# Kernel optimization log

Measured on AMD Instinct MI355X. Metric: run time of the kernel, lower is better.

Reference implementation:

```python
import jax, jax.numpy as jnp
import numpy as np

NUM_NODES = 50000

def setup_inputs() -> dict:
    key = jax.random.key(0)
    k1, k2 = jax.random.split(key)
    x = jax.random.normal(k1, (NUM_NODES, 64), dtype=jnp.float32)
    edge_index = jax.random.randint(k2, (2, 800000), 0, NUM_NODES, dtype=jnp.int64)
    return {"x": x, "edge_index": edge_index}

def reference(x, edge_index):
    # gather source-node features along edges, scatter-mean into target nodes
    row, col = edge_index[0], edge_index[1]
    num_nodes = x.shape[0]
    gathered = x[row]  # [E, D]
    summed = jax.ops.segment_sum(gathered, col, num_segments=num_nodes)  # [N, D]
    count = jax.ops.segment_sum(jnp.ones_like(col, dtype=x.dtype), col, num_segments=num_nodes)  # [N]
    # mean with divide-by-zero guard (matches torch_geometric scatter reduce='mean')
    out = summed / jnp.maximum(count, 1.0)[:, None]
    return out
```

## Files before the change

### kernel.cpp

```cpp
#include <hip/hip_runtime.h>

#define N_NODES 50000
#define DIM 64
#define NPB 32
#define NB 1563
#define NCHUNK 128
#define CAPB 1024
#define CAP 1024

typedef unsigned short ushort_t;

__device__ __forceinline__ ushort_t f32_to_bf16(float f) {
    unsigned u = __float_as_uint(f);
    u += 0x7FFFu + ((u >> 16) & 1u);
    return (ushort_t)(u >> 16);
}

__device__ __forceinline__ void acc_pair(float& a0, float& a1, unsigned u) {
    a0 += __uint_as_float(u << 16);
    a1 += __uint_as_float(u & 0xFFFF0000u);
}

__global__ void convert_hist_kernel(const float* __restrict__ xf,
                                    ushort_t* __restrict__ xh,
                                    const int* __restrict__ col,
                                    int* __restrict__ localH,
                                    int E, int chunk, int n4) {
    __shared__ int h[NB];
    int c = blockIdx.x;
    int tid = threadIdx.x;
    for (int i = c * blockDim.x + tid; i < n4; i += gridDim.x * blockDim.x) {
        float4 v = *reinterpret_cast<const float4*>(xf + (size_t)i * 4);
        ushort4 hh;
        hh.x = f32_to_bf16(v.x);
        hh.y = f32_to_bf16(v.y);
        hh.z = f32_to_bf16(v.z);
        hh.w = f32_to_bf16(v.w);
        *reinterpret_cast<ushort4*>(xh + (size_t)i * 4) = hh;
    }
    for (int b = tid; b < NB; b += blockDim.x) h[b] = 0;
    __syncthreads();
    int beg = c * chunk, end = min(beg + chunk, E);
    int nfull = (end - beg) >> 2;
    for (int g = tid; g < nfull; g += blockDim.x) {
        int4 c4 = *reinterpret_cast<const int4*>(col + beg + g * 4);
        atomicAdd(&h[c4.x >> 5], 1);
        atomicAdd(&h[c4.y >> 5], 1);
        atomicAdd(&h[c4.z >> 5], 1);
        atomicAdd(&h[c4.w >> 5], 1);
    }
    for (int e = beg + nfull * 4 + tid; e < end; e += blockDim.x)
        atomicAdd(&h[col[e] >> 5], 1);
    __syncthreads();
    for (int b = tid; b < NB; b += blockDim.x)
        localH[(size_t)c * NB + b] = h[b];
}

__global__ void chunk_offset_kernel(int* __restrict__ localH,
                                    int* __restrict__ bucket_total) {
    int b = blockIdx.x;
    int lane = threadIdx.x;
    int running = 0;
    #pragma unroll
    for (int c0 = 0; c0 < NCHUNK; c0 += 64) {
        int c = c0 + lane;
        int v = localH[(size_t)c * NB + b];
        int incl = v;
        #pragma unroll
        for (int ofs = 1; ofs < 64; ofs <<= 1) {
            int t = __shfl_up(incl, ofs);
            if (lane >= ofs) incl += t;
        }
        localH[(size_t)c * NB + b] = running + incl - v;
        running += __shfl(incl, 63);
    }
    if (lane == 0) bucket_total[b] = running;
}

__global__ void binning_kernel(const int* __restrict__ row,
                               const int* __restrict__ col,
                               const int* __restrict__ localH,
                               unsigned* __restrict__ packed,
                               int E, int chunk) {
    __shared__ int cursor[NB];
    int c = blockIdx.x;
    int tid = threadIdx.x;
    for (int b = tid; b < NB; b += blockDim.x)
        cursor[b] = b * CAPB + localH[(size_t)c * NB + b];
    __syncthreads();
    int beg = c * chunk, end = min(beg + chunk, E);
    int nfull = (end - beg) >> 2;
    for (int g = tid; g < nfull; g += blockDim.x) {
        int e = beg + g * 4;
        int4 d4 = *reinterpret_cast<const int4*>(col + e);
        int4 s4 = *reinterpret_cast<const int4*>(row + e);
        int p0 = atomicAdd(&cursor[d4.x >> 5], 1);
        packed[p0] = (unsigned)s4.x | ((unsigned)(d4.x & 31) << 16);
        int p1 = atomicAdd(&cursor[d4.y >> 5], 1);
        packed[p1] = (unsigned)s4.y | ((unsigned)(d4.y & 31) << 16);
        int p2 = atomicAdd(&cursor[d4.z >> 5], 1);
        packed[p2] = (unsigned)s4.z | ((unsigned)(d4.z & 31) << 16);
        int p3 = atomicAdd(&cursor[d4.w >> 5], 1);
        packed[p3] = (unsigned)s4.w | ((unsigned)(d4.w & 31) << 16);
    }
    for (int e = beg + nfull * 4 + tid; e < end; e += blockDim.x) {
        int d = col[e];
        int p = atomicAdd(&cursor[d >> 5], 1);
        packed[p] = (unsigned)row[e] | ((unsigned)(d & 31) << 16);
    }
}

template <bool BF16>
__global__ __launch_bounds__(512)
void aggregate_bucket_kernel(const float* __restrict__ xf,
                             const ushort_t* __restrict__ xh,
                             const unsigned* __restrict__ packed,
                             const int* __restrict__ bucket_total,
                             float* __restrict__ out) {
    __shared__ unsigned buf[CAP];
    __shared__ unsigned short srcs[CAP];
    __shared__ int hist[NPB];
    __shared__ int segoff[NPB];
    __shared__ int cursor[NPB];
    __shared__ int cnt_tot[NPB];

    int b = blockIdx.x;
    int tid = threadIdx.x;
    int lane = tid & 63;
    int wv = tid >> 6;
    int g8 = lane >> 3;
    int o = lane & 7;
    int seg_beg = b * CAPB;
    int seg_end = seg_beg + bucket_total[b];
    int node_base = b * NPB;
    int nnodes = min(NPB, N_NODES - node_base);

    float acc[4][8];
    #pragma unroll
    for (int r = 0; r < 4; ++r)
        #pragma unroll
        for (int k = 0; k < 8; ++k) acc[r][k] = 0.0f;
    if (tid < NPB) cnt_tot[tid] = 0;

    for (int cs = seg_beg; cs < seg_end; cs += CAP) {
        int m = min(CAP, seg_end - cs);
        __syncthreads();
        if (tid < NPB) hist[tid] = 0;
        __syncthreads();
        for (int i = tid; i < m; i += 512) {
            unsigned v = packed[cs + i];
            buf[i] = v;
            atomicAdd(&hist[v >> 16], 1);
        }
        __syncthreads();
        if (tid < NPB) {
            int v = hist[tid];
            int incl = v;
            #pragma unroll
            for (int ofs = 1; ofs < 32; ofs <<= 1) {
                int t = __shfl_up(incl, ofs);
                if (lane >= ofs) incl += t;
            }
            segoff[tid] = incl - v;
            cursor[tid] = incl - v;
            cnt_tot[tid] += v;
        }
        __syncthreads();
        for (int i = tid; i < m; i += 512) {
            unsigned v = buf[i];
            int p = atomicAdd(&cursor[v >> 16], 1);
            srcs[p] = (unsigned short)(v & 0xFFFF);
        }
        __syncthreads();
        #pragma unroll
        for (int r = 0; r < 4; ++r) {
            int ln = wv * 4 + r;
            int st = segoff[ln];
            int len = hist[ln];
            int j = 0;
            for (; j + 16 <= len; j += 16) {
                int s0 = srcs[st + j + g8];
                int s1 = srcs[st + j + 8 + g8];
                if (BF16) {
                    uint4 a0 = *reinterpret_cast<const uint4*>(xh + (size_t)s0 * DIM + o * 8);
                    uint4 a1 = *reinterpret_cast<const uint4*>(xh + (size_t)s1 * DIM + o * 8);
                    acc_pair(acc[r][0], acc[r][1], a0.x);
                    acc_pair(acc[r][2], acc[r][3], a0.y);
                    acc_pair(acc[r][4], acc[r][5], a0.z);
                    acc_pair(acc[r][6], acc[r][7], a0.w);
                    acc_pair(acc[r][0], acc[r][1], a1.x);
                    acc_pair(acc[r][2], acc[r][3], a1.y);
                    acc_pair(acc[r][4], acc[r][5], a1.z);
                    acc_pair(acc[r][6], acc[r][7], a1.w);
                } else {
                    float4 u0 = *reinterpret_cast<const float4*>(xf + (size_t)s0 * DIM + o * 8);
                    float4 u1 = *reinterpret_cast<const float4*>(xf + (size_t)s0 * DIM + o * 8 + 4);
                    float4 u2 = *reinterpret_cast<const float4*>(xf + (size_t)s1 * DIM + o * 8);
                    float4 u3 = *reinterpret_cast<const float4*>(xf + (size_t)s1 * DIM + o * 8 + 4);
                    acc[r][0] += u0.x + u2.x; acc[r][1] += u0.y + u2.y;
                    acc[r][2] += u0.z + u2.z; acc[r][3] += u0.w + u2.w;
                    acc[r][4] += u1.x + u3.x; acc[r][5] += u1.y + u3.y;
                    acc[r][6] += u1.z + u3.z; acc[r][7] += u1.w + u3.w;
                }
            }
            for (; j < len; j += 8) {
                if (j + g8 < len) {
                    int s = srcs[st + j + g8];
                    if (BF16) {
                        uint4 a0 = *reinterpret_cast<const uint4*>(xh + (size_t)s * DIM + o * 8);
                        acc_pair(acc[r][0], acc[r][1], a0.x);
                        acc_pair(acc[r][2], acc[r][3], a0.y);
                        acc_pair(acc[r][4], acc[r][5], a0.z);
                        acc_pair(acc[r][6], acc[r][7], a0.w);
                    } else {
                        float4 u0 = *reinterpret_cast<const float4*>(xf + (size_t)s * DIM + o * 8);
                        float4 u1 = *reinterpret_cast<const float4*>(xf + (size_t)s * DIM + o * 8 + 4);
                        acc[r][0] += u0.x; acc[r][1] += u0.y;
                        acc[r][2] += u0.z; acc[r][3] += u0.w;
                        acc[r][4] += u1.x; acc[r][5] += u1.y;
                        acc[r][6] += u1.z; acc[r][7] += u1.w;
                    }
                }
            }
        }
    }
    __syncthreads();
    #pragma unroll
    for (int r = 0; r < 4; ++r) {
        int ln = wv * 4 + r;
        #pragma unroll
        for (int k = 0; k < 8; ++k) {
            acc[r][k] += __shfl_xor(acc[r][k], 8);
            acc[r][k] += __shfl_xor(acc[r][k], 16);
            acc[r][k] += __shfl_xor(acc[r][k], 32);
        }
        if (g8 == 0 && ln < nnodes) {
            int c = cnt_tot[ln];
            float inv = (c > 0) ? 1.0f / (float)c : 0.0f;
            float4 lo = make_float4(acc[r][0] * inv, acc[r][1] * inv,
                                    acc[r][2] * inv, acc[r][3] * inv);
            float4 hi = make_float4(acc[r][4] * inv, acc[r][5] * inv,
                                    acc[r][6] * inv, acc[r][7] * inv);
            float* op = out + (size_t)(node_base + ln) * DIM + o * 8;
            *reinterpret_cast<float4*>(op) = lo;
            *reinterpret_cast<float4*>(op + 4) = hi;
        }
    }
}

extern "C" void kernel_launch(void* const* d_in, const int* in_sizes, int n_in,
                              void* d_out, int out_size, void* d_ws, size_t ws_size,
                              hipStream_t stream) {
    const float* x = (const float*)d_in[0];
    const int* edge_index = (const int*)d_in[1];
    int E = in_sizes[1] / 2;
    const int* row = edge_index;
    const int* col = edge_index + E;
    float* out = (float*)d_out;

    int chunk = (((E + NCHUNK - 1) / NCHUNK) + 3) & ~3;
    int n4 = N_NODES * DIM / 4;

    int* bucket_total = (int*)d_ws;
    int* localH       = bucket_total + 1568;
    unsigned* packed  = (unsigned*)(localH + (size_t)NCHUNK * NB);
    ushort_t* xh      = (ushort_t*)(packed + (size_t)NB * CAPB);
    size_t need_bf16  = (size_t)((char*)(xh + (size_t)N_NODES * DIM) - (char*)d_ws);
    bool use_bf16 = (ws_size >= need_bf16);

    convert_hist_kernel<<<NCHUNK, 1024, 0, stream>>>(x, xh, col, localH, E, chunk,
                                                     use_bf16 ? n4 : 0);
    chunk_offset_kernel<<<NB, 64, 0, stream>>>(localH, bucket_total);
    binning_kernel<<<NCHUNK, 1024, 0, stream>>>(row, col, localH, packed, E, chunk);
    if (use_bf16)
        aggregate_bucket_kernel<true><<<NB, 512, 0, stream>>>(x, xh, packed, bucket_total, out);
    else
        aggregate_bucket_kernel<false><<<NB, 512, 0, stream>>>(x, xh, packed, bucket_total, out);
}
```

Before: 60.03 us.

## Replace chunk-offset scan with global atomic cursor reservation in binning

Removes the separate per-chunk histogram write and the column-wise prefix scan kernel. Each binning block now builds its local histogram itself and reserves contiguous ranges per bucket with one global atomicAdd per nonzero bucket. The aggregate kernel reads the final cursor as the segment end. This cuts a kernel launch and the localH round trip, and the chunk count is doubled. Slot order within a bucket becomes nondeterministic, which can change float summation order, and the col array is now read twice inside one kernel.

```diff
diff --git a/kernel.cpp b/kernel.cpp
--- a/kernel.cpp
+++ b/kernel.cpp
@@ -4,7 +4,7 @@
 #define DIM 64
 #define NPB 32
 #define NB 1563
-#define NCHUNK 128
+#define NCHUNK 256
 #define CAPB 1024
 #define CAP 1024
 
@@ -21,15 +21,12 @@
     a1 += __uint_as_float(u & 0xFFFF0000u);
 }
 
-__global__ void convert_hist_kernel(const float* __restrict__ xf,
+__global__ void convert_init_kernel(const float* __restrict__ xf,
                                     ushort_t* __restrict__ xh,
-                                    const int* __restrict__ col,
-                                    int* __restrict__ localH,
-                                    int E, int chunk, int n4) {
-    __shared__ int h[NB];
-    int c = blockIdx.x;
-    int tid = threadIdx.x;
-    for (int i = c * blockDim.x + tid; i < n4; i += gridDim.x * blockDim.x) {
+                                    int* __restrict__ cursor, int n4) {
+    int gt = blockIdx.x * blockDim.x + threadIdx.x;
+    if (gt <= NB) cursor[gt] = gt * CAPB;
+    for (int i = gt; i < n4; i += gridDim.x * blockDim.x) {
         float4 v = *reinterpret_cast<const float4*>(xf + (size_t)i * 4);
         ushort4 hh;
         hh.x = f32_to_bf16(v.x);
@@ -38,6 +35,17 @@
         hh.w = f32_to_bf16(v.w);
         *reinterpret_cast<ushort4*>(xh + (size_t)i * 4) = hh;
     }
+}
+
+__global__ void binning_kernel(const int* __restrict__ row,
+                               const int* __restrict__ col,
+                               int* __restrict__ cursor,
+                               unsigned* __restrict__ packed,
+                               int E, int chunk) {
+    __shared__ int h[NB];
+    __shared__ int lcur[NB];
+    int c = blockIdx.x;
+    int tid = threadIdx.x;
     for (int b = tid; b < NB; b += blockDim.x) h[b] = 0;
     __syncthreads();
     int beg = c * chunk, end = min(beg + chunk, E);
@@ -52,60 +60,27 @@
     for (int e = beg + nfull * 4 + tid; e < end; e += blockDim.x)
         atomicAdd(&h[col[e] >> 5], 1);
     __syncthreads();
-    for (int b = tid; b < NB; b += blockDim.x)
-        localH[(size_t)c * NB + b] = h[b];
-}
-
-__global__ void chunk_offset_kernel(int* __restrict__ localH,
-                                    int* __restrict__ bucket_total) {
-    int b = blockIdx.x;
-    int lane = threadIdx.x;
-    int running = 0;
-    #pragma unroll
-    for (int c0 = 0; c0 < NCHUNK; c0 += 64) {
-        int c = c0 + lane;
-        int v = localH[(size_t)c * NB + b];
-        int incl = v;
-        #pragma unroll
-        for (int ofs = 1; ofs < 64; ofs <<= 1) {
-            int t = __shfl_up(incl, ofs);
-            if (lane >= ofs) incl += t;
-        }
-        localH[(size_t)c * NB + b] = running + incl - v;
-        running += __shfl(incl, 63);
-    }
-    if (lane == 0) bucket_total[b] = running;
-}
-
-__global__ void binning_kernel(const int* __restrict__ row,
-                               const int* __restrict__ col,
-                               const int* __restrict__ localH,
-                               unsigned* __restrict__ packed,
-                               int E, int chunk) {
-    __shared__ int cursor[NB];
-    int c = blockIdx.x;
-    int tid = threadIdx.x;
-    for (int b = tid; b < NB; b += blockDim.x)
-        cursor[b] = b * CAPB + localH[(size_t)c * NB + b];
-    __syncthreads();
-    int beg = c * chunk, end = min(beg + chunk, E);
-    int nfull = (end - beg) >> 2;
+    for (int b = tid; b < NB; b += blockDim.x) {
+        int v = h[b];
+        lcur[b] = (v > 0) ? atomicAdd(&cursor[b], v) : 0;
+    }
+    __syncthreads();
     for (int g = tid; g < nfull; g += blockDim.x) {
         int e = beg + g * 4;
         int4 d4 = *reinterpret_cast<const int4*>(col + e);
         int4 s4 = *reinterpret_cast<const int4*>(row + e);
-        int p0 = atomicAdd(&cursor[d4.x >> 5], 1);
+        int p0 = atomicAdd(&lcur[d4.x >> 5], 1);
         packed[p0] = (unsigned)s4.x | ((unsigned)(d4.x & 31) << 16);
-        int p1 = atomicAdd(&cursor[d4.y >> 5], 1);
+        int p1 = atomicAdd(&lcur[d4.y >> 5], 1);
         packed[p1] = (unsigned)s4.y | ((unsigned)(d4.y & 31) << 16);
-        int p2 = atomicAdd(&cursor[d4.z >> 5], 1);
+        int p2 = atomicAdd(&lcur[d4.z >> 5], 1);
         packed[p2] = (unsigned)s4.z | ((unsigned)(d4.z & 31) << 16);
-        int p3 = atomicAdd(&cursor[d4.w >> 5], 1);
+        int p3 = atomicAdd(&lcur[d4.w >> 5], 1);
         packed[p3] = (unsigned)s4.w | ((unsigned)(d4.w & 31) << 16);
     }
     for (int e = beg + nfull * 4 + tid; e < end; e += blockDim.x) {
         int d = col[e];
-        int p = atomicAdd(&cursor[d >> 5], 1);
+        int p = atomicAdd(&lcur[d >> 5], 1);
         packed[p] = (unsigned)row[e] | ((unsigned)(d & 31) << 16);
     }
 }
@@ -115,13 +90,13 @@
 void aggregate_bucket_kernel(const float* __restrict__ xf,
                              const ushort_t* __restrict__ xh,
                              const unsigned* __restrict__ packed,
-                             const int* __restrict__ bucket_total,
+                             const int* __restrict__ cursor,
                              float* __restrict__ out) {
     __shared__ unsigned buf[CAP];
     __shared__ unsigned short srcs[CAP];
     __shared__ int hist[NPB];
     __shared__ int segoff[NPB];
-    __shared__ int cursor[NPB];
+    __shared__ int lcur[NPB];
     __shared__ int cnt_tot[NPB];
 
     int b = blockIdx.x;
@@ -131,7 +106,7 @@
     int g8 = lane >> 3;
     int o = lane & 7;
     int seg_beg = b * CAPB;
-    int seg_end = seg_beg + bucket_total[b];
+    int seg_end = cursor[b];
     int node_base = b * NPB;
     int nnodes = min(NPB, N_NODES - node_base);
 
@@ -162,13 +137,13 @@
                 if (lane >= ofs) incl += t;
             }
             segoff[tid] = incl - v;
-            cursor[tid] = incl - v;
+            lcur[tid] = incl - v;
             cnt_tot[tid] += v;
         }
         __syncthreads();
         for (int i = tid; i < m; i += 512) {
             unsigned v = buf[i];
-            int p = atomicAdd(&cursor[v >> 16], 1);
+            int p = atomicAdd(&lcur[v >> 16], 1);
             srcs[p] = (unsigned short)(v & 0xFFFF);
         }
         __syncthreads();
@@ -261,19 +236,16 @@
     int chunk = (((E + NCHUNK - 1) / NCHUNK) + 3) & ~3;
     int n4 = N_NODES * DIM / 4;
 
-    int* bucket_total = (int*)d_ws;
-    int* localH       = bucket_total + 1568;
-    unsigned* packed  = (unsigned*)(localH + (size_t)NCHUNK * NB);
-    ushort_t* xh      = (ushort_t*)(packed + (size_t)NB * CAPB);
-    size_t need_bf16  = (size_t)((char*)(xh + (size_t)N_NODES * DIM) - (char*)d_ws);
+    int* cursor      = (int*)d_ws;
+    unsigned* packed = (unsigned*)(cursor + 1568);
+    ushort_t* xh     = (ushort_t*)(packed + (size_t)NB * CAPB);
+    size_t need_bf16 = (size_t)((char*)(xh + (size_t)N_NODES * DIM) - (char*)d_ws);
     bool use_bf16 = (ws_size >= need_bf16);
 
-    convert_hist_kernel<<<NCHUNK, 1024, 0, stream>>>(x, xh, col, localH, E, chunk,
-                                                     use_bf16 ? n4 : 0);
-    chunk_offset_kernel<<<NB, 64, 0, stream>>>(localH, bucket_total);
-    binning_kernel<<<NCHUNK, 1024, 0, stream>>>(row, col, localH, packed, E, chunk);
+    convert_init_kernel<<<256, 1024, 0, stream>>>(x, xh, cursor, use_bf16 ? n4 : 0);
+    binning_kernel<<<NCHUNK, 1024, 0, stream>>>(row, col, cursor, packed, E, chunk);
     if (use_bf16)
-        aggregate_bucket_kernel<true><<<NB, 512, 0, stream>>>(x, xh, packed, bucket_total, out);
+        aggregate_bucket_kernel<true><<<NB, 512, 0, stream>>>(x, xh, packed, cursor, out);
     else
-        aggregate_bucket_kernel<false><<<NB, 512, 0, stream>>>(x, xh, packed, bucket_total, out);
-}
+        aggregate_bucket_kernel<false><<<NB, 512, 0, stream>>>(x, xh, packed, cursor, out);
+}
```

Measured after the change: 58.41 us. -2.7%, faster.
